# Performance work log

Measured on AMD Instinct MI355X. Metric: run time of the kernel, lower is better.

Reference implementation:

```python
import jax, jax.numpy as jnp
import numpy as np

N_NODES = 150000
N_EDGES = 4800000
IN_DIM, HID_DIM, OUT_DIM = 1433, 16, 7


def setup_inputs() -> dict:
    key = jax.random.key(0)
    ks = jax.random.split(key, 8)
    features = jax.random.normal(ks[0], (N_NODES, IN_DIM), dtype=jnp.float32)
    edge_src = jax.random.randint(ks[1], (N_EDGES,), 0, N_NODES, dtype=jnp.int32)
    edge_dst = jax.random.randint(ks[2], (N_EDGES,), 0, N_NODES, dtype=jnp.int32)
    adj_vals = jax.random.uniform(ks[3], (N_EDGES,), dtype=jnp.float32)
    W1 = jax.random.normal(ks[4], (IN_DIM, HID_DIM), dtype=jnp.float32) * (1.0 / np.sqrt(IN_DIM))
    b1 = jnp.zeros((HID_DIM,), dtype=jnp.float32)
    W2 = jax.random.normal(ks[5], (HID_DIM, OUT_DIM), dtype=jnp.float32) * (1.0 / np.sqrt(HID_DIM))
    b2 = jnp.zeros((OUT_DIM,), dtype=jnp.float32)
    return {"features": features, "edge_src": edge_src, "edge_dst": edge_dst,
            "adj_vals": adj_vals, "W1": W1, "b1": b1, "W2": W2, "b2": b2}


def _gcn_layer(x, edge_src, edge_dst, adj_vals, W, b):
    # h = A_hat @ (x @ W) + b ; dense transform first since in_dim >= out_dim
    xw = x @ W                                   # [N, d_out]
    msg = adj_vals[:, None] * xw[edge_src]       # [E, d_out] gather
    agg = jax.ops.segment_sum(msg, edge_dst, num_segments=x.shape[0])  # scatter-add
    return agg + b


def reference(features, edge_src, edge_dst, adj_vals, W1, b1, W2, b2):
    h1 = jax.nn.relu(_gcn_layer(features, edge_src, edge_dst, adj_vals, W1, b1))
    # dropout in original forward is a no-op (result discarded) -> omitted
    h2 = _gcn_layer(h1, edge_src, edge_dst, adj_vals, W2, b2)
    return jax.nn.log_softmax(h2, axis=1)
```

## Files before the change

kernel.cpp:

```cpp
#include <hip/hip_runtime.h>
#include <float.h>
#include <stdint.h>

#define IN_DIM 1433
#define HID 16
#define OUTD 7

#define AS1 __attribute__((address_space(1)))
#define AS3 __attribute__((address_space(3)))

__global__ __launch_bounds__(256, 4) void gemm1_kernel(
    const float* __restrict__ feat, const float* __restrict__ W1,
    float* __restrict__ xw1, int N)
{
    __shared__ float xs[4][2][64 * 16];
    const int t = threadIdx.x;
    const int l = t & 63;
    const int w = t >> 6;
    const int row0 = blockIdx.x * 256;
    const int h = __builtin_amdgcn_readfirstlane((4 - w) & 3);
    const long maxBase = (long)N * IN_DIM - 4;

    const int R = row0 + 4 * l + w;

    long src[4];
#pragma unroll
    for (int j = 0; j < 4; ++j) {
        const int rc = j * 16 + (l >> 2);
        const int bs = (l & 3) ^ (rc & 3);
        src[j] = (long)(row0 + 4 * rc + w) * IN_DIM + h + 4 * bs;
    }

    float acc[16];
#pragma unroll
    for (int j = 0; j < 16; ++j) acc[j] = 0.f;

    for (int k = 0; k < h; ++k) {
        const float x = (R < N) ? feat[(long)R * IN_DIM + k] : 0.f;
        const float* wr = W1 + k * HID;
#pragma unroll
        for (int j = 0; j < 16; ++j) acc[j] += x * wr[j];
    }
    asm volatile("s_waitcnt vmcnt(0)" ::: "memory");
    __builtin_amdgcn_sched_barrier(0);

    auto stage = [&](int buf, int i) {
#pragma unroll
        for (int j = 0; j < 4; ++j) {
            long e = src[j] + 16 * i;
            if (e > maxBase) e = maxBase;
            __builtin_amdgcn_global_load_lds(
                (const AS1 void*)(feat + e),
                (AS3 void*)(&xs[w][buf][j * 256]), 16, 0, 0);
        }
    };

#define WAITVM(Nimm)                                                         \
    asm volatile("s_waitcnt vmcnt(" #Nimm ")" ::: "memory");                 \
    __builtin_amdgcn_sched_barrier(0);

    const int lx = l & 3;
#define COMPUTE_FULL(buf, i)                                                 \
    {                                                                        \
        const float* xrow = &xs[w][buf][l * 16];                             \
        const int kb0 = h + 16 * (i);                                        \
        _Pragma("unroll")                                                    \
        for (int b = 0; b < 4; ++b) {                                        \
            const float4 xv = *(const float4*)&xrow[((b ^ lx) << 2)];        \
            const float* wk = W1 + (size_t)(kb0 + 4 * b) * HID;              \
            _Pragma("unroll")                                                \
            for (int e = 0; e < 4; ++e) {                                    \
                const float xe = ((const float*)&xv)[e];                     \
                const float4 wA = *(const float4*)(wk + e * HID);            \
                const float4 wB = *(const float4*)(wk + e * HID + 4);        \
                const float4 wC = *(const float4*)(wk + e * HID + 8);        \
                const float4 wD = *(const float4*)(wk + e * HID + 12);       \
                acc[0]  += xe * wA.x; acc[1]  += xe * wA.y;                  \
                acc[2]  += xe * wA.z; acc[3]  += xe * wA.w;                  \
                acc[4]  += xe * wB.x; acc[5]  += xe * wB.y;                  \
                acc[6]  += xe * wB.z; acc[7]  += xe * wB.w;                  \
                acc[8]  += xe * wC.x; acc[9]  += xe * wC.y;                  \
                acc[10] += xe * wC.z; acc[11] += xe * wC.w;                  \
                acc[12] += xe * wD.x; acc[13] += xe * wD.y;                  \
                acc[14] += xe * wD.z; acc[15] += xe * wD.w;                  \
            }                                                                \
        }                                                                    \
    }

    stage(0, 0);
    stage(1, 1);
    for (int i = 0; i < 88; ++i) {
        WAITVM(4);
        COMPUTE_FULL(i & 1, i);
        stage(i & 1, i + 2);
    }
    WAITVM(4);
    COMPUTE_FULL(0, 88);
    WAITVM(0);
    {
        const int kl = 9 - h;
        const int nb = kl >> 2, tl = kl & 3;
        const float* xrow = &xs[w][1][l * 16];
        const int kb0 = h + 16 * 89;
        for (int b = 0; b < nb; ++b) {
            const float4 xv = *(const float4*)&xrow[((b ^ lx) << 2)];
            const float* wk = W1 + (size_t)(kb0 + 4 * b) * HID;
#pragma unroll
            for (int e = 0; e < 4; ++e) {
                const float xe = ((const float*)&xv)[e];
                const float* wr = wk + e * HID;
#pragma unroll
                for (int j = 0; j < 16; ++j) acc[j] += xe * wr[j];
            }
        }
        for (int kk = nb * 4; kk < nb * 4 + tl; ++kk) {
            const float x = xrow[(((kk >> 2) ^ lx) << 2) | (kk & 3)];
            const float* wr = W1 + (size_t)(kb0 + kk) * HID;
#pragma unroll
            for (int j = 0; j < 16; ++j) acc[j] += x * wr[j];
        }
    }
#undef COMPUTE_FULL
#undef WAITVM

    if (R < N) {
        float4* o = (float4*)(xw1 + (size_t)R * HID);
        o[0] = make_float4(acc[0],  acc[1],  acc[2],  acc[3]);
        o[1] = make_float4(acc[4],  acc[5],  acc[6],  acc[7]);
        o[2] = make_float4(acc[8],  acc[9],  acc[10], acc[11]);
        o[3] = make_float4(acc[12], acc[13], acc[14], acc[15]);
    }
}

__global__ __launch_bounds__(256) void hist_kernel(
    const int* __restrict__ dst, int* __restrict__ cnt, int E)
{
    const int i4 = blockIdx.x * 256 + threadIdx.x;
    const int e0 = i4 * 4;
    if (e0 + 3 < E) {
        const int4 d = ((const int4*)dst)[i4];
        atomicAdd(&cnt[d.x], 1);
        atomicAdd(&cnt[d.y], 1);
        atomicAdd(&cnt[d.z], 1);
        atomicAdd(&cnt[d.w], 1);
    } else {
        for (int e = e0; e < E; ++e) atomicAdd(&cnt[dst[e]], 1);
    }
}

__global__ __launch_bounds__(256) void scan1_kernel(
    const int* __restrict__ cnt, int* __restrict__ offs,
    int* __restrict__ bsum, int N)
{
    __shared__ int lds[256];
    const int t = threadIdx.x, b = blockIdx.x;
    const int base = b * 1024 + t * 4;
    int c0 = 0, c1 = 0, c2 = 0, c3 = 0;
    if (base + 0 < N) c0 = cnt[base + 0];
    if (base + 1 < N) c1 = cnt[base + 1];
    if (base + 2 < N) c2 = cnt[base + 2];
    if (base + 3 < N) c3 = cnt[base + 3];
    const int s = c0 + c1 + c2 + c3;
    lds[t] = s;
    __syncthreads();
    for (int off = 1; off < 256; off <<= 1) {
        int v = (t >= off) ? lds[t - off] : 0;
        __syncthreads();
        lds[t] += v;
        __syncthreads();
    }
    const int excl = lds[t] - s;
    if (t == 255) bsum[b] = lds[255];
    int run = excl;
    if (base + 0 < N) { offs[base + 0] = run; run += c0; }
    if (base + 1 < N) { offs[base + 1] = run; run += c1; }
    if (base + 2 < N) { offs[base + 2] = run; run += c2; }
    if (base + 3 < N) { offs[base + 3] = run; run += c3; }
}

__global__ __launch_bounds__(256) void scan2_kernel(
    const int* __restrict__ bsum, int* __restrict__ bbase, int NB)
{
    __shared__ int lds[256];
    const int t = threadIdx.x;
    const int v = (t < NB) ? bsum[t] : 0;
    lds[t] = v;
    __syncthreads();
    for (int off = 1; off < 256; off <<= 1) {
        int u = (t >= off) ? lds[t - off] : 0;
        __syncthreads();
        lds[t] += u;
        __syncthreads();
    }
    bbase[t] = lds[t] - v;
}

__global__ __launch_bounds__(256) void scan3_kernel(
    int* __restrict__ offs, int* __restrict__ cursor,
    const int* __restrict__ bbase, int N, int E)
{
    const int t = threadIdx.x, b = blockIdx.x;
    const int add = bbase[b];
    const int base = b * 1024 + t * 4;
#pragma unroll
    for (int i = 0; i < 4; ++i) {
        const int idx = base + i;
        if (idx < N) {
            const int v = offs[idx] + add;
            offs[idx] = v;
            cursor[idx] = v;
        }
    }
    if (b == 0 && t == 0) offs[N] = E;
}

__global__ __launch_bounds__(256) void fill_kernel(
    const int* __restrict__ src, const int* __restrict__ dst,
    const float* __restrict__ a, int* __restrict__ cursor,
    uint2* __restrict__ pairs, int E)
{
    const int i4 = blockIdx.x * 256 + threadIdx.x;
    const int e0 = i4 * 4;
    if (e0 + 3 < E) {
        const int4   s4 = ((const int4*)src)[i4];
        const int4   d4 = ((const int4*)dst)[i4];
        const float4 a4 = ((const float4*)a)[i4];
        int p0 = atomicAdd(&cursor[d4.x], 1);
        pairs[p0] = make_uint2((unsigned)s4.x, __float_as_uint(a4.x));
        int p1 = atomicAdd(&cursor[d4.y], 1);
        pairs[p1] = make_uint2((unsigned)s4.y, __float_as_uint(a4.y));
        int p2 = atomicAdd(&cursor[d4.z], 1);
        pairs[p2] = make_uint2((unsigned)s4.z, __float_as_uint(a4.z));
        int p3 = atomicAdd(&cursor[d4.w], 1);
        pairs[p3] = make_uint2((unsigned)s4.w, __float_as_uint(a4.w));
    } else {
        for (int e = e0; e < E; ++e) {
            const int pos = atomicAdd(&cursor[dst[e]], 1);
            pairs[pos] = make_uint2((unsigned)src[e], __float_as_uint(a[e]));
        }
    }
}

__global__ __launch_bounds__(256) void gather1_kernel(
    const uint2* __restrict__ pairs, const int* __restrict__ offs,
    const float* __restrict__ xw1, const float* __restrict__ b1,
    const float* __restrict__ W2, float* __restrict__ xw2, int N)
{
    __shared__ float w2s[HID * OUTD];
    const int t = threadIdx.x;
    if (t < HID * OUTD) w2s[t] = W2[t];
    __syncthreads();
    const int lane = t & 63;
    const int r = blockIdx.x * 4 + (t >> 6);
    if (r >= N) return;
    const int g = lane >> 2;
    const int c = lane & 3;
    const int start = offs[r], end = offs[r + 1];
    float4 acc = make_float4(0.f, 0.f, 0.f, 0.f);
    int e = start + g;
    for (; e + 16 < end; e += 32) {
        const uint2 p0 = pairs[e];
        const uint2 p1 = pairs[e + 16];
        const float4 v0 = *(const float4*)(xw1 + (size_t)p0.x * HID + c * 4);
        const float4 v1 = *(const float4*)(xw1 + (size_t)p1.x * HID + c * 4);
        const float a0 = __uint_as_float(p0.y);
        const float a1 = __uint_as_float(p1.y);
        acc.x += a0 * v0.x + a1 * v1.x;
        acc.y += a0 * v0.y + a1 * v1.y;
        acc.z += a0 * v0.z + a1 * v1.z;
        acc.w += a0 * v0.w + a1 * v1.w;
    }
    if (e < end) {
        const uint2 p0 = pairs[e];
        const float4 v0 = *(const float4*)(xw1 + (size_t)p0.x * HID + c * 4);
        const float a0 = __uint_as_float(p0.y);
        acc.x += a0 * v0.x; acc.y += a0 * v0.y;
        acc.z += a0 * v0.z; acc.w += a0 * v0.w;
    }
#pragma unroll
    for (int m = 4; m < 64; m <<= 1) {
        acc.x += __shfl_xor(acc.x, m);
        acc.y += __shfl_xor(acc.y, m);
        acc.z += __shfl_xor(acc.z, m);
        acc.w += __shfl_xor(acc.w, m);
    }
    const float4 b1v = ((const float4*)b1)[c];
    float4 hv;
    hv.x = fmaxf(acc.x + b1v.x, 0.f);
    hv.y = fmaxf(acc.y + b1v.y, 0.f);
    hv.z = fmaxf(acc.z + b1v.z, 0.f);
    hv.w = fmaxf(acc.w + b1v.w, 0.f);
    float hh[16];
#pragma unroll
    for (int cc = 0; cc < 4; ++cc) {
        hh[cc * 4 + 0] = __shfl(hv.x, cc);
        hh[cc * 4 + 1] = __shfl(hv.y, cc);
        hh[cc * 4 + 2] = __shfl(hv.z, cc);
        hh[cc * 4 + 3] = __shfl(hv.w, cc);
    }
    const int col = (lane & 7) < OUTD ? (lane & 7) : 0;
    float sacc = 0.f;
#pragma unroll
    for (int j = 0; j < HID; ++j) sacc += hh[j] * w2s[j * OUTD + col];
    if (lane < 8) xw2[(size_t)r * 8 + lane] = (lane < OUTD) ? sacc : 0.f;
}

__global__ __launch_bounds__(256) void gather2_kernel(
    const uint2* __restrict__ pairs, const int* __restrict__ offs,
    const float* __restrict__ xw2, const float* __restrict__ b2,
    float* __restrict__ out, int N)
{
    const int t = threadIdx.x;
    const int lane = t & 63;
    const int r = blockIdx.x * 4 + (t >> 6);
    if (r >= N) return;
    const int g = lane >> 1;
    const int c = lane & 1;
    const int start = offs[r], end = offs[r + 1];
    float4 acc = make_float4(0.f, 0.f, 0.f, 0.f);
    for (int e = start + g; e < end; e += 32) {
        const uint2 p = pairs[e];
        const float4 v = *(const float4*)(xw2 + (size_t)p.x * 8 + c * 4);
        const float a = __uint_as_float(p.y);
        acc.x += a * v.x; acc.y += a * v.y;
        acc.z += a * v.z; acc.w += a * v.w;
    }
#pragma unroll
    for (int m = 2; m < 64; m <<= 1) {
        acc.x += __shfl_xor(acc.x, m);
        acc.y += __shfl_xor(acc.y, m);
        acc.z += __shfl_xor(acc.z, m);
        acc.w += __shfl_xor(acc.w, m);
    }
    float4 x;
    if (c == 0) {
        const float4 b2v = *(const float4*)b2;
        x.x = acc.x + b2v.x; x.y = acc.y + b2v.y;
        x.z = acc.z + b2v.z; x.w = acc.w + b2v.w;
    } else {
        x.x = acc.x + b2[4]; x.y = acc.y + b2[5];
        x.z = acc.z + b2[6]; x.w = -FLT_MAX;
    }
    float mymax = fmaxf(fmaxf(x.x, x.y), x.z);
    if (c == 0) mymax = fmaxf(mymax, x.w);
    const float m = fmaxf(mymax, __shfl_xor(mymax, 1));
    float es = expf(x.x - m) + expf(x.y - m) + expf(x.z - m);
    if (c == 0) es += expf(x.w - m);
    const float s = es + __shfl_xor(es, 1);
    const float lg = logf(s);
    float* op = out + (size_t)r * OUTD;
    if (c == 0) {
        op[0] = x.x - m - lg; op[1] = x.y - m - lg;
        op[2] = x.z - m - lg; op[3] = x.w - m - lg;
    } else {
        op[4] = x.x - m - lg; op[5] = x.y - m - lg;
        op[6] = x.z - m - lg;
    }
}

extern "C" void kernel_launch(void* const* d_in, const int* in_sizes, int n_in,
                              void* d_out, int out_size, void* d_ws, size_t ws_size,
                              hipStream_t stream)
{
    const float* feat  = (const float*)d_in[0];
    const int*   esrc  = (const int*)d_in[1];
    const int*   edst  = (const int*)d_in[2];
    const float* avals = (const float*)d_in[3];
    const float* W1    = (const float*)d_in[4];
    const float* b1    = (const float*)d_in[5];
    const float* W2    = (const float*)d_in[6];
    const float* b2    = (const float*)d_in[7];
    float* out = (float*)d_out;

    const int N = in_sizes[0] / IN_DIM;
    const int E = in_sizes[1];
    const int NB = (N + 1023) / 1024;

    char* p = (char*)d_ws;
    float* xw1   = (float*)p; p += (size_t)N * HID * sizeof(float);
    float* xw2   = (float*)p; p += (size_t)N * 8 * sizeof(float);
    int*   cnt   = (int*)p;   p += (size_t)N * sizeof(int);
    int*   offs  = (int*)p;   p += (size_t)(N + 1) * sizeof(int);
    int*   cursor= (int*)p;   p += (size_t)N * sizeof(int);
    int*   bsum  = (int*)p;   p += 256 * sizeof(int);
    int*   bbase = (int*)p;   p += 256 * sizeof(int);
    p = (char*)(((uintptr_t)p + 15) & ~(uintptr_t)15);
    uint2* pairs = (uint2*)p;

    hipMemsetAsync(cnt, 0, (size_t)N * sizeof(int), stream);

    gemm1_kernel<<<(N + 255) / 256, 256, 0, stream>>>(feat, W1, xw1, N);

    {
        const int n4 = (E + 3) / 4;
        hist_kernel<<<(n4 + 255) / 256, 256, 0, stream>>>(edst, cnt, E);
    }
    scan1_kernel<<<NB, 256, 0, stream>>>(cnt, offs, bsum, N);
    scan2_kernel<<<1, 256, 0, stream>>>(bsum, bbase, NB);
    scan3_kernel<<<NB, 256, 0, stream>>>(offs, cursor, bbase, N, E);
    {
        const int n4 = (E + 3) / 4;
        fill_kernel<<<(n4 + 255) / 256, 256, 0, stream>>>(esrc, edst, avals, cursor, pairs, E);
    }

    gather1_kernel<<<(N + 3) / 4, 256, 0, stream>>>(pairs, offs, xw1, b1, W2, xw2, N);
    gather2_kernel<<<(N + 3) / 4, 256, 0, stream>>>(pairs, offs, xw2, b2, out, N);
}
```

Before: 954.6 us.

## Split GEMM1 K dimension across two wave groups and reduce through LDS

Doubles the gemm1 block to 512 threads. Each row's 1433-wide dot product is split into two K halves handled by separate wave groups, and the partial sums are combined through shared memory before the store. The aim is more memory-level parallelism and shorter serial pipelines per wave in this bandwidth-bound GEMM. In exchange it doubles LDS per block (64KB), adds a __syncthreads, and may reduce the number of resident blocks.

```diff
diff --git a/kernel.cpp b/kernel.cpp
--- a/kernel.cpp
+++ b/kernel.cpp
@@ -9,45 +9,54 @@
 #define AS1 __attribute__((address_space(1)))
 #define AS3 __attribute__((address_space(3)))
 
-__global__ __launch_bounds__(256, 4) void gemm1_kernel(
+__global__ __launch_bounds__(512, 4) void gemm1_kernel(
     const float* __restrict__ feat, const float* __restrict__ W1,
     float* __restrict__ xw1, int N)
 {
-    __shared__ float xs[4][2][64 * 16];
+    __shared__ float xs[8][2][64 * 16];
     const int t = threadIdx.x;
     const int l = t & 63;
-    const int w = t >> 6;
+    const int w = __builtin_amdgcn_readfirstlane(t >> 6);
+    const int c  = w & 3;
+    const int hf = w >> 2;
     const int row0 = blockIdx.x * 256;
-    const int h = __builtin_amdgcn_readfirstlane((4 - w) & 3);
+    const int R = row0 + 4 * l + c;
     const long maxBase = (long)N * IN_DIM - 4;
 
-    const int R = row0 + 4 * l + w;
+    const int h    = (4 - c) & 3;
+    const int sc   = 716 + h;
+    const int kbeg = hf ? sc : h;
+    const int rem  = hf ? (13 - h) : 12;
+    const int nb   = rem >> 2;
+    const int tl   = rem & 3;
 
     long src[4];
 #pragma unroll
     for (int j = 0; j < 4; ++j) {
         const int rc = j * 16 + (l >> 2);
         const int bs = (l & 3) ^ (rc & 3);
-        src[j] = (long)(row0 + 4 * rc + w) * IN_DIM + h + 4 * bs;
+        src[j] = (long)(row0 + 4 * rc + c) * IN_DIM + kbeg + 4 * bs;
     }
 
     float acc[16];
 #pragma unroll
     for (int j = 0; j < 16; ++j) acc[j] = 0.f;
 
-    for (int k = 0; k < h; ++k) {
-        const float x = (R < N) ? feat[(long)R * IN_DIM + k] : 0.f;
-        const float* wr = W1 + k * HID;
-#pragma unroll
-        for (int j = 0; j < 16; ++j) acc[j] += x * wr[j];
+    if (hf == 0) {
+        for (int k = 0; k < h; ++k) {
+            const float x = (R < N) ? feat[(long)R * IN_DIM + k] : 0.f;
+            const float* wr = W1 + k * HID;
+#pragma unroll
+            for (int j = 0; j < 16; ++j) acc[j] += x * wr[j];
+        }
     }
     asm volatile("s_waitcnt vmcnt(0)" ::: "memory");
     __builtin_amdgcn_sched_barrier(0);
 
-    auto stage = [&](int buf, int i) {
+    auto stage = [&](int buf, int tile) {
 #pragma unroll
         for (int j = 0; j < 4; ++j) {
-            long e = src[j] + 16 * i;
+            long e = src[j] + 16 * tile;
             if (e > maxBase) e = maxBase;
             __builtin_amdgcn_global_load_lds(
                 (const AS1 void*)(feat + e),
@@ -60,10 +69,10 @@
     __builtin_amdgcn_sched_barrier(0);
 
     const int lx = l & 3;
-#define COMPUTE_FULL(buf, i)                                                 \
+#define COMP_FULL(buf, i)                                                    \
     {                                                                        \
         const float* xrow = &xs[w][buf][l * 16];                             \
-        const int kb0 = h + 16 * (i);                                        \
+        const int kb0 = kbeg + 16 * (i);                                     \
         _Pragma("unroll")                                                    \
         for (int b = 0; b < 4; ++b) {                                        \
             const float4 xv = *(const float4*)&xrow[((b ^ lx) << 2)];        \
@@ -89,19 +98,17 @@
 
     stage(0, 0);
     stage(1, 1);
-    for (int i = 0; i < 88; ++i) {
+    for (int i = 0; i < 43; ++i) {
         WAITVM(4);
-        COMPUTE_FULL(i & 1, i);
+        COMP_FULL(i & 1, i);
         stage(i & 1, i + 2);
     }
     WAITVM(4);
-    COMPUTE_FULL(0, 88);
+    COMP_FULL(1, 43);
     WAITVM(0);
     {
-        const int kl = 9 - h;
-        const int nb = kl >> 2, tl = kl & 3;
-        const float* xrow = &xs[w][1][l * 16];
-        const int kb0 = h + 16 * 89;
+        const float* xrow = &xs[w][0][l * 16];
+        const int kb0 = kbeg + 704;
         for (int b = 0; b < nb; ++b) {
             const float4 xv = *(const float4*)&xrow[((b ^ lx) << 2)];
             const float* wk = W1 + (size_t)(kb0 + 4 * b) * HID;
@@ -120,15 +127,26 @@
             for (int j = 0; j < 16; ++j) acc[j] += x * wr[j];
         }
     }
-#undef COMPUTE_FULL
+#undef COMP_FULL
 #undef WAITVM
 
-    if (R < N) {
-        float4* o = (float4*)(xw1 + (size_t)R * HID);
-        o[0] = make_float4(acc[0],  acc[1],  acc[2],  acc[3]);
-        o[1] = make_float4(acc[4],  acc[5],  acc[6],  acc[7]);
-        o[2] = make_float4(acc[8],  acc[9],  acc[10], acc[11]);
-        o[3] = make_float4(acc[12], acc[13], acc[14], acc[15]);
+    if (hf == 1) {
+        float* s = &xs[w][0][l * 16];
+#pragma unroll
+        for (int j = 0; j < 16; ++j) s[j] = acc[j];
+    }
+    __syncthreads();
+    if (hf == 0) {
+        const float* s = &xs[w + 4][0][l * 16];
+#pragma unroll
+        for (int j = 0; j < 16; ++j) acc[j] += s[j];
+        if (R < N) {
+            float4* o = (float4*)(xw1 + (size_t)R * HID);
+            o[0] = make_float4(acc[0],  acc[1],  acc[2],  acc[3]);
+            o[1] = make_float4(acc[4],  acc[5],  acc[6],  acc[7]);
+            o[2] = make_float4(acc[8],  acc[9],  acc[10], acc[11]);
+            o[3] = make_float4(acc[12], acc[13], acc[14], acc[15]);
+        }
     }
 }
 
@@ -389,7 +407,7 @@
 
     hipMemsetAsync(cnt, 0, (size_t)N * sizeof(int), stream);
 
-    gemm1_kernel<<<(N + 255) / 256, 256, 0, stream>>>(feat, W1, xw1, N);
+    gemm1_kernel<<<(N + 255) / 256, 512, 0, stream>>>(feat, W1, xw1, N);
 
     {
         const int n4 = (E + 3) / 4;
```

After: 973.0 us. Within noise of the previous version (+1.9%).
